# Optimization experiments

Hardware: AMD Instinct MI355X
Metric: run time of the kernel (lower is better)

## Reference

```python
import jax, jax.numpy as jnp
import numpy as np

S, B, C, HD = 3, 64, 256, 256
ZS, XS = 7, 31
EPS = 1e-5


def _bn(x, g, b, m, v):
    # inference-mode BatchNorm2d on NCHW
    inv = g / jnp.sqrt(v + EPS)
    return x * inv[None, :, None, None] + (b - m * inv)[None, :, None, None]


def _dw3(x, w):
    # depthwise 3x3 conv, VALID padding, groups = channels; w: [C,1,3,3]
    return jax.lax.conv_general_dilated(
        x, w, (1, 1), 'VALID', feature_group_count=x.shape[1],
        dimension_numbers=('NCHW', 'OIHW', 'NCHW'))


def _xcorr_depthwise(x, k):
    # Siamese depthwise cross-correlation: groups = batch*channels
    b, c, h, w = x.shape
    o = jax.lax.conv_general_dilated(
        x.reshape(1, b * c, h, w),
        k.reshape(b * c, 1, k.shape[2], k.shape[3]),
        (1, 1), 'VALID', feature_group_count=b * c,
        dimension_numbers=('NCHW', 'OIHW', 'NCHW'))
    return o.reshape(b, c, o.shape[2], o.shape[3])


def _c1(x, w):
    # 1x1 conv, no bias; w: [O,C]
    return jnp.einsum('bchw,oc->bohw', x, w)


def _forward(z_fs, x_fs, pre_w, pre_g, pre_b, pre_m, pre_v,
             head_w, head_g, head_b, head_m, head_v,
             cls_w1, cls_g, cls_b, cls_m, cls_v, cls_w2, cls_b2,
             loc_w1, loc_g, loc_b, loc_m, loc_v, loc_w2, loc_b2,
             ctr_w1, ctr_g, ctr_b, ctr_m, ctr_v, ctr_w2, ctr_b2,
             w_cls, w_loc, w_ctr):
    relu = jax.nn.relu
    cls_l, loc_l, ctr_l = [], [], []
    for i in range(S):
        search = relu(_bn(_dw3(x_fs[i], pre_w[i]), pre_g[i], pre_b[i], pre_m[i], pre_v[i]))
        kernel = relu(_bn(_dw3(z_fs[i], pre_w[i]), pre_g[i], pre_b[i], pre_m[i], pre_v[i]))
        feat = relu(_bn(_c1(_xcorr_depthwise(search, kernel), head_w[i]),
                        head_g[i], head_b[i], head_m[i], head_v[i]))

        def hd(w1, g, b, m, v, w2, b2):
            h = relu(_bn(_c1(feat, w1), g, b, m, v))
            return _c1(h, w2) + b2[None, :, None, None]

        cls_l.append(hd(cls_w1[i], cls_g[i], cls_b[i], cls_m[i], cls_v[i], cls_w2[i], cls_b2[i]))
        loc_l.append(hd(loc_w1[i], loc_g[i], loc_b[i], loc_m[i], loc_v[i], loc_w2[i], loc_b2[i]))
        ctr_l.append(hd(ctr_w1[i], ctr_g[i], ctr_b[i], ctr_m[i], ctr_v[i], ctr_w2[i], ctr_b2[i]))

    wc = jax.nn.softmax(w_cls)
    wl = jax.nn.softmax(w_loc)
    wt = jax.nn.softmax(w_ctr)
    cls = sum(cls_l[i] * wc[i] for i in range(S))
    loc = sum(loc_l[i] * wl[i] for i in range(S))
    ctr = sum(ctr_l[i] * wt[i] for i in range(S))
    return cls, loc, ctr


def setup_inputs() -> dict:
    key = jax.random.key(0)
    ks = iter(jax.random.split(key, 64))

    def rn(shape, scale=0.05):
        return jax.random.normal(next(ks), shape, jnp.float32) * scale

    def bn_params(n):
        return (jnp.ones((S, n), jnp.float32), jnp.zeros((S, n), jnp.float32),
                rn((S, n), 0.1), jax.random.uniform(next(ks), (S, n), jnp.float32) + 0.5)

    inp = {}
    inp['z_fs'] = rn((S, B, C, ZS, ZS), 1.0)
    inp['x_fs'] = rn((S, B, C, XS, XS), 1.0)
    inp['pre_w'] = rn((S, C, 1, 3, 3), 0.2)
    inp['pre_g'], inp['pre_b'], inp['pre_m'], inp['pre_v'] = bn_params(C)
    inp['head_w'] = rn((S, HD, C))
    inp['head_g'], inp['head_b'], inp['head_m'], inp['head_v'] = bn_params(HD)
    for nm, co in (('cls', 2), ('loc', 4), ('ctr', 1)):
        inp[nm + '_w1'] = rn((S, HD, HD))
        inp[nm + '_g'], inp[nm + '_b'], inp[nm + '_m'], inp[nm + '_v'] = bn_params(HD)
        inp[nm + '_w2'] = rn((S, co, HD))
        inp[nm + '_b2'] = jnp.zeros((S, co), jnp.float32)
    inp['w_cls'] = jnp.ones((S,), jnp.float32)
    inp['w_loc'] = jnp.ones((S,), jnp.float32)
    inp['w_ctr'] = jnp.ones((S,), jnp.float32)
    return inp


def reference(z_fs, x_fs, pre_w, pre_g, pre_b, pre_m, pre_v,
              head_w, head_g, head_b, head_m, head_v,
              cls_w1, cls_g, cls_b, cls_m, cls_v, cls_w2, cls_b2,
              loc_w1, loc_g, loc_b, loc_m, loc_v, loc_w2, loc_b2,
              ctr_w1, ctr_g, ctr_b, ctr_m, ctr_v, ctr_w2, ctr_b2,
              w_cls, w_loc, w_ctr):
    return _forward(z_fs, x_fs, pre_w, pre_g, pre_b, pre_m, pre_v,
                    head_w, head_g, head_b, head_m, head_v,
                    cls_w1, cls_g, cls_b, cls_m, cls_v, cls_w2, cls_b2,
                    loc_w1, loc_g, loc_b, loc_m, loc_v, loc_w2, loc_b2,
                    ctr_w1, ctr_g, ctr_b, ctr_m, ctr_v, ctr_w2, ctr_b2,
                    w_cls, w_loc, w_ctr)
```

## Files before the change

### kernel.cpp

```cpp
#include <hip/hip_runtime.h>
#include <hip/hip_bf16.h>

using bf16 = __hip_bfloat16;

#define B_  64
#define C_  256
#define HD_ 256
#define XS  31
#define XO  29
#define ZS  7
#define ZO  5
#define OSP 25
#define XO2 (XO*XO)
#define ZO2 (ZO*ZO)
#define OS2 (OSP*OSP)
#define EPSF 1e-5f

#define XCST 976
#define SRS  36
#define SCST (29 * SRS)

typedef __attribute__((ext_vector_type(4))) float f32x4;
typedef __attribute__((ext_vector_type(8))) short s16x8;

__device__ __forceinline__ unsigned short f2bf(float f) {
    union { float f; unsigned int u; } a; a.f = f;
    unsigned int r = a.u + 0x7FFF + ((a.u >> 16) & 1);
    return (unsigned short)(r >> 16);
}
__device__ __forceinline__ unsigned int pk2(unsigned short a, unsigned short b) {
    return (unsigned int)a | ((unsigned int)b << 16);
}

__global__ void wconv_k(const float* __restrict__ hw, const float* __restrict__ cw,
                        const float* __restrict__ lw, const float* __restrict__ tw,
                        unsigned short* __restrict__ o)
{
    int i = blockIdx.x * 256 + threadIdx.x;
    if (i >= 4 * 196608) return;
    int seg = i / 196608, r = i - seg * 196608;
    const float* s = (seg == 0) ? hw : (seg == 1) ? cw : (seg == 2) ? lw : tw;
    o[i] = f2bf(s[r]);
}

__global__ __launch_bounds__(256) void fused_pre_xcorr(
    const float* __restrict__ x, const float* __restrict__ z,
    const float* __restrict__ w, const float* __restrict__ g,
    const float* __restrict__ bb, const float* __restrict__ mm,
    const float* __restrict__ vv, unsigned short* __restrict__ out,
    int si_base)
{
    const int zs  = blockIdx.y;
    const int si  = si_base + zs;
    const int bc0 = blockIdx.x * 2;
    const int tid = threadIdx.x;

    __shared__ float xt[2 * XCST + 8];
    __shared__ float st[2 * SCST + 16];
    __shared__ float zt[2 * 49];
    __shared__ float ktl[2 * 25];
    __shared__ float wtl[2 * 9];
    __shared__ float sprm[4];

    const float* xp = x + ((size_t)si * B_ * C_ + bc0) * (XS * XS);
    #pragma unroll
    for (int k2 = 0; k2 < 8; ++k2) {
        int idx = tid + k2 * 256;
        if (idx < 2 * XS * XS) {
            int off = idx + (idx >= XS * XS ? (XCST - XS * XS) : 0);
            xt[off] = xp[idx];
        }
    }
    if (tid < 98) zt[tid] = z[((size_t)si * B_ * C_ + bc0) * 49 + tid];
    if (tid < 18) wtl[tid] = w[((size_t)si * C_ + (bc0 & (C_ - 1))) * 9 + tid];
    if (tid < 2) {
        int cg = si * C_ + (bc0 & (C_ - 1)) + tid;
        float iv = g[cg] * rsqrtf(vv[cg] + EPSF);
        sprm[tid * 2]     = iv;
        sprm[tid * 2 + 1] = bb[cg] - mm[cg] * iv;
    }
    __syncthreads();

    if (tid < 50) {
        int ch = (tid >= 25) ? 1 : 0;
        int l  = tid - ch * 25;
        int oy = l / 5, ox = l - (l / 5) * 5;
        const float* zb = &zt[ch * 49];
        const float* wb = &wtl[ch * 9];
        float a = 0.f;
        #pragma unroll
        for (int dy = 0; dy < 3; ++dy)
            #pragma unroll
            for (int dx = 0; dx < 3; ++dx)
                a += zb[(oy + dy) * ZS + ox + dx] * wb[dy * 3 + dx];
        ktl[ch * 25 + l] = fmaxf(a * sprm[ch * 2] + sprm[ch * 2 + 1], 0.f);
    }

    if (tid < 240) {
        int ch    = (tid >= 120) ? 1 : 0;
        int rem   = tid - ch * 120;
        int strip = rem >> 3;
        int cgp   = rem & 7;
        int r0    = strip * 2;
        const float* base = &xt[ch * XCST + r0 * XS + cgp * 4];
        const float* wb   = &wtl[ch * 9];
        float w0 = wb[0], w1 = wb[1], w2 = wb[2],
              w3 = wb[3], w4 = wb[4], w5 = wb[5],
              w6 = wb[6], w7 = wb[7], w8 = wb[8];
        const float inv  = sprm[ch * 2];
        const float beta = sprm[ch * 2 + 1];

        float a0 = 0.f, a1 = 0.f, a2 = 0.f, a3 = 0.f;
        float b0 = 0.f, b1 = 0.f, b2 = 0.f, b3 = 0.f;
        #pragma unroll
        for (int dy = 0; dy < 4; ++dy) {
            const float* rp = base + dy * XS;
            float v0 = rp[0], v1 = rp[1], v2 = rp[2],
                  v3 = rp[3], v4 = rp[4], v5 = rp[5];
            if (dy < 3) {
                float u0 = (dy == 0) ? w0 : (dy == 1) ? w3 : w6;
                float u1 = (dy == 0) ? w1 : (dy == 1) ? w4 : w7;
                float u2 = (dy == 0) ? w2 : (dy == 1) ? w5 : w8;
                a0 += v0 * u0 + v1 * u1 + v2 * u2;
                a1 += v1 * u0 + v2 * u1 + v3 * u2;
                a2 += v2 * u0 + v3 * u1 + v4 * u2;
                a3 += v3 * u0 + v4 * u1 + v5 * u2;
            }
            if (dy >= 1) {
                float u0 = (dy == 1) ? w0 : (dy == 2) ? w3 : w6;
                float u1 = (dy == 1) ? w1 : (dy == 2) ? w4 : w7;
                float u2 = (dy == 1) ? w2 : (dy == 2) ? w5 : w8;
                b0 += v0 * u0 + v1 * u1 + v2 * u2;
                b1 += v1 * u0 + v2 * u1 + v3 * u2;
                b2 += v2 * u0 + v3 * u1 + v4 * u2;
                b3 += v3 * u0 + v4 * u1 + v5 * u2;
            }
        }
        float4 ra;
        ra.x = fmaxf(a0 * inv + beta, 0.f);
        ra.y = fmaxf(a1 * inv + beta, 0.f);
        ra.z = fmaxf(a2 * inv + beta, 0.f);
        ra.w = fmaxf(a3 * inv + beta, 0.f);
        *(float4*)&st[ch * SCST + r0 * SRS + cgp * 4] = ra;
        if (r0 + 1 < XO) {
            float4 rb;
            rb.x = fmaxf(b0 * inv + beta, 0.f);
            rb.y = fmaxf(b1 * inv + beta, 0.f);
            rb.z = fmaxf(b2 * inv + beta, 0.f);
            rb.w = fmaxf(b3 * inv + beta, 0.f);
            *(float4*)&st[ch * SCST + (r0 + 1) * SRS + cgp * 4] = rb;
        }
    }
    __syncthreads();

    {
        const int ch = tid >> 7;
        const int l  = tid & 127;
        if (l < 125) {
            const float* kb = &ktl[ch * 25];
            float kt[25];
            #pragma unroll
            for (int j = 0; j < 25; ++j) kt[j] = kb[j];
            int u  = l / 5;
            int v0 = (l - u * 5) * 5;
            const float* sbase = &st[ch * SCST + u * SRS + v0];
            float o0 = 0.f, o1 = 0.f, o2 = 0.f, o3 = 0.f, o4 = 0.f;
            #pragma unroll
            for (int p = 0; p < 5; ++p) {
                const float* rp = sbase + p * SRS;
                float r0 = rp[0], r1 = rp[1], r2 = rp[2], r3 = rp[3], r4 = rp[4],
                      r5 = rp[5], r6 = rp[6], r7 = rp[7], r8 = rp[8];
                float k0 = kt[p * 5], k1 = kt[p * 5 + 1], k2 = kt[p * 5 + 2],
                      k3 = kt[p * 5 + 3], k4 = kt[p * 5 + 4];
                o0 += r0 * k0 + r1 * k1 + r2 * k2 + r3 * k3 + r4 * k4;
                o1 += r1 * k0 + r2 * k1 + r3 * k2 + r4 * k3 + r5 * k4;
                o2 += r2 * k0 + r3 * k1 + r4 * k2 + r5 * k3 + r6 * k4;
                o3 += r3 * k0 + r4 * k1 + r5 * k2 + r6 * k3 + r7 * k4;
                o4 += r4 * k0 + r5 * k1 + r6 * k2 + r7 * k3 + r8 * k4;
            }
            unsigned short* op = out + ((size_t)zs * B_ * C_ + bc0 + ch) * OS2
                                     + u * OSP + v0;
            op[0] = f2bf(o0); op[1] = f2bf(o1); op[2] = f2bf(o2);
            op[3] = f2bf(o3); op[4] = f2bf(o4);
        }
    }
}

__global__ __launch_bounds__(256) void c1_mfma(
    const unsigned short* __restrict__ X,
    const float* __restrict__ W,
    const unsigned short* __restrict__ Wbf,
    const float* __restrict__ g, const float* __restrict__ bb,
    const float* __restrict__ mm, const float* __restrict__ vv,
    unsigned short* __restrict__ out, int si_base)
{
    __shared__ unsigned short Abuf[4 * 128 * 8];
    __shared__ unsigned short Bbuf[4 * 128 * 8];
    __shared__ float s_inv[128], s_beta[128];

    const int tid  = threadIdx.x;
    const int wave = tid >> 6, lane = tid & 63;
    const int quad = lane >> 4, l16 = lane & 15;
    const int sb = blockIdx.x * 128;
    const int ob = blockIdx.y * 128;
    const int zs = blockIdx.z >> 6;
    const int si = si_base + zs;
    const int b  = blockIdx.z & 63;
    const int wm = (wave & 1) * 64, wn = (wave >> 1) * 64;

    const float* gs  = g  + (size_t)si * HD_;
    const float* bbs = bb + (size_t)si * HD_;
    const float* mms = mm + (size_t)si * HD_;
    const float* vvs = vv + (size_t)si * HD_;
    const float* Ws  = W  + (size_t)si * HD_ * C_;
    const unsigned short* Wbs = Wbf ? Wbf + (size_t)si * HD_ * C_ : nullptr;

    if (tid < 128) {
        int o = ob + tid;
        float iv = gs[o] * rsqrtf(vvs[o] + EPSF);
        s_inv[tid]  = iv;
        s_beta[tid] = bbs[o] - mms[o] * iv;
    }

    const int sm = tid & 127;
    const int kh = tid >> 7;
    const unsigned short* Xb = X + ((size_t)zs * B_ + b) * C_ * OS2;
    const bool npred = (sb + sm) < OS2;

    f32x4 acc[4][4];
    #pragma unroll
    for (int i = 0; i < 4; ++i)
        #pragma unroll
        for (int j = 0; j < 4; ++j)
            acc[i][j] = (f32x4){0.f, 0.f, 0.f, 0.f};

    for (int kk = 0; kk < C_; kk += 32) {
        uint4 pa0, pa1;
        if (Wbs) {
            const unsigned short* wp = Wbs + (size_t)(ob + sm) * C_ + kk + kh * 16;
            pa0 = *(const uint4*)(wp);
            pa1 = *(const uint4*)(wp + 8);
        } else {
            const float* wp = Ws + (size_t)(ob + sm) * C_ + kk + kh * 16;
            float4 w0 = *(const float4*)(wp + 0);
            float4 w1 = *(const float4*)(wp + 4);
            float4 w2 = *(const float4*)(wp + 8);
            float4 w3 = *(const float4*)(wp + 12);
            pa0.x = pk2(f2bf(w0.x), f2bf(w0.y)); pa0.y = pk2(f2bf(w0.z), f2bf(w0.w));
            pa0.z = pk2(f2bf(w1.x), f2bf(w1.y)); pa0.w = pk2(f2bf(w1.z), f2bf(w1.w));
            pa1.x = pk2(f2bf(w2.x), f2bf(w2.y)); pa1.y = pk2(f2bf(w2.z), f2bf(w2.w));
            pa1.z = pk2(f2bf(w3.x), f2bf(w3.y)); pa1.w = pk2(f2bf(w3.z), f2bf(w3.w));
        }
        *(uint4*)&Abuf[((kh * 2 + 0) * 128 + sm) * 8] = pa0;
        *(uint4*)&Abuf[((kh * 2 + 1) * 128 + sm) * 8] = pa1;

        unsigned short bu[16];
        #pragma unroll
        for (int j = 0; j < 16; ++j)
            bu[j] = npred ? Xb[(size_t)(kk + kh * 16 + j) * OS2 + sb + sm]
                          : (unsigned short)0;
        uint4 pb0, pb1;
        pb0.x = pk2(bu[0],  bu[1]);  pb0.y = pk2(bu[2],  bu[3]);
        pb0.z = pk2(bu[4],  bu[5]);  pb0.w = pk2(bu[6],  bu[7]);
        pb1.x = pk2(bu[8],  bu[9]);  pb1.y = pk2(bu[10], bu[11]);
        pb1.z = pk2(bu[12], bu[13]); pb1.w = pk2(bu[14], bu[15]);
        *(uint4*)&Bbuf[((kh * 2 + 0) * 128 + sm) * 8] = pb0;
        *(uint4*)&Bbuf[((kh * 2 + 1) * 128 + sm) * 8] = pb1;

        __syncthreads();

        s16x8 af[4], bfr[4];
        #pragma unroll
        for (int mt = 0; mt < 4; ++mt)
            af[mt] = *(const s16x8*)&Abuf[(quad * 128 + wm + mt * 16 + l16) * 8];
        #pragma unroll
        for (int nt = 0; nt < 4; ++nt)
            bfr[nt] = *(const s16x8*)&Bbuf[(quad * 128 + wn + nt * 16 + l16) * 8];
        #pragma unroll
        for (int mt = 0; mt < 4; ++mt)
            #pragma unroll
            for (int nt = 0; nt < 4; ++nt)
                acc[mt][nt] = __builtin_amdgcn_mfma_f32_16x16x32_bf16(
                    af[mt], bfr[nt], acc[mt][nt], 0, 0, 0);

        __syncthreads();
    }

    #pragma unroll
    for (int mt = 0; mt < 4; ++mt) {
        #pragma unroll
        for (int r = 0; r < 4; ++r) {
            int orow = wm + mt * 16 + quad * 4 + r;
            float iv = s_inv[orow], be = s_beta[orow];
            size_t obase = (((size_t)zs * B_ + b) * HD_ + (ob + orow)) * OS2;
            #pragma unroll
            for (int nt = 0; nt < 4; ++nt) {
                int s = sb + wn + nt * 16 + l16;
                if (s < OS2)
                    out[obase + s] = f2bf(fmaxf(acc[mt][nt][r] * iv + be, 0.f));
            }
        }
    }
}

__global__ __launch_bounds__(256) void heads3_mfma(
    const unsigned short* __restrict__ feat,
    const float* __restrict__ w1c, const float* __restrict__ w1l, const float* __restrict__ w1t,
    const unsigned short* __restrict__ Wbf,
    const float* __restrict__ gc, const float* __restrict__ bc2, const float* __restrict__ mc, const float* __restrict__ vc,
    const float* __restrict__ gl, const float* __restrict__ bl, const float* __restrict__ ml, const float* __restrict__ vl,
    const float* __restrict__ gt, const float* __restrict__ bt, const float* __restrict__ mt2, const float* __restrict__ vt,
    const float* __restrict__ w2c, const float* __restrict__ w2l, const float* __restrict__ w2t,
    const float* __restrict__ wvc, const float* __restrict__ wvl, const float* __restrict__ wvt,
    int si_base, float* __restrict__ oacc)
{
    __shared__ unsigned short Abuf[4 * 128 * 8];
    __shared__ unsigned short Bbuf[4 * 128 * 8];
    __shared__ float s_inv[128], s_beta[128];
    __shared__ float s_w2[4 * 256];

    const int tid  = threadIdx.x;
    const int wave = tid >> 6, lane = tid & 63;
    const int quad = lane >> 4, l16 = lane & 15;
    const int sb   = blockIdx.x * 128;
    const int by   = blockIdx.y;
    const int head = by >> 1;
    const int lob  = (by & 1) * 128;
    const int zs   = blockIdx.z >> 6;
    const int si   = si_base + zs;
    const int b    = blockIdx.z & 63;
    const int wm = (wave & 1) * 64, wn = (wave >> 1) * 64;

    const float* W  = (head == 0) ? w1c : (head == 1) ? w1l : w1t;
    const float* g  = (head == 0) ? gc  : (head == 1) ? gl  : gt;
    const float* bb = (head == 0) ? bc2 : (head == 1) ? bl  : bt;
    const float* mm = (head == 0) ? mc  : (head == 1) ? ml  : mt2;
    const float* vv = (head == 0) ? vc  : (head == 1) ? vl  : vt;
    const float* w2 = (head == 0) ? w2c : (head == 1) ? w2l : w2t;
    const float* wv = (head == 0) ? wvc : (head == 1) ? wvl : wvt;
    const int  CON  = (head == 0) ? 2 : (head == 1) ? 4 : 1;

    const float* Ws  = W + (size_t)si * HD_ * C_;
    const unsigned short* Wbs =
        Wbf ? Wbf + (size_t)(head + 1) * (3 * HD_ * C_) + (size_t)si * HD_ * C_ : nullptr;
    g  += (size_t)si * HD_;  bb += (size_t)si * HD_;
    mm += (size_t)si * HD_;  vv += (size_t)si * HD_;
    w2 += (size_t)si * CON * HD_;

    if (tid < 128) {
        int o = lob + tid;
        float iv = g[o] * rsqrtf(vv[o] + EPSF);
        s_inv[tid]  = iv;
        s_beta[tid] = bb[o] - mm[o] * iv;
    }
    for (int t = tid; t < CON * 256; t += 256) s_w2[t] = w2[t];

    const int sm = tid & 127;
    const int kh = tid >> 7;
    const unsigned short* Xb = feat + ((size_t)zs * B_ + b) * C_ * OS2;
    const bool npred = (sb + sm) < OS2;

    f32x4 acc[4][4];
    #pragma unroll
    for (int i = 0; i < 4; ++i)
        #pragma unroll
        for (int j = 0; j < 4; ++j)
            acc[i][j] = (f32x4){0.f, 0.f, 0.f, 0.f};

    for (int kk = 0; kk < C_; kk += 32) {
        uint4 pa0, pa1;
        if (Wbs) {
            const unsigned short* wp = Wbs + (size_t)(lob + sm) * C_ + kk + kh * 16;
            pa0 = *(const uint4*)(wp);
            pa1 = *(const uint4*)(wp + 8);
        } else {
            const float* wp = Ws + (size_t)(lob + sm) * C_ + kk + kh * 16;
            float4 w0 = *(const float4*)(wp + 0);
            float4 w1 = *(const float4*)(wp + 4);
            float4 w2v4 = *(const float4*)(wp + 8);
            float4 w3 = *(const float4*)(wp + 12);
            pa0.x = pk2(f2bf(w0.x), f2bf(w0.y)); pa0.y = pk2(f2bf(w0.z), f2bf(w0.w));
            pa0.z = pk2(f2bf(w1.x), f2bf(w1.y)); pa0.w = pk2(f2bf(w1.z), f2bf(w1.w));
            pa1.x = pk2(f2bf(w2v4.x), f2bf(w2v4.y)); pa1.y = pk2(f2bf(w2v4.z), f2bf(w2v4.w));
            pa1.z = pk2(f2bf(w3.x), f2bf(w3.y)); pa1.w = pk2(f2bf(w3.z), f2bf(w3.w));
        }
        *(uint4*)&Abuf[((kh * 2 + 0) * 128 + sm) * 8] = pa0;
        *(uint4*)&Abuf[((kh * 2 + 1) * 128 + sm) * 8] = pa1;

        unsigned short bu[16];
        #pragma unroll
        for (int j = 0; j < 16; ++j)
            bu[j] = npred ? Xb[(size_t)(kk + kh * 16 + j) * OS2 + sb + sm]
                          : (unsigned short)0;
        uint4 pb0, pb1;
        pb0.x = pk2(bu[0],  bu[1]);  pb0.y = pk2(bu[2],  bu[3]);
        pb0.z = pk2(bu[4],  bu[5]);  pb0.w = pk2(bu[6],  bu[7]);
        pb1.x = pk2(bu[8],  bu[9]);  pb1.y = pk2(bu[10], bu[11]);
        pb1.z = pk2(bu[12], bu[13]); pb1.w = pk2(bu[14], bu[15]);
        *(uint4*)&Bbuf[((kh * 2 + 0) * 128 + sm) * 8] = pb0;
        *(uint4*)&Bbuf[((kh * 2 + 1) * 128 + sm) * 8] = pb1;

        __syncthreads();

        s16x8 af[4], bfr[4];
        #pragma unroll
        for (int mt = 0; mt < 4; ++mt)
            af[mt] = *(const s16x8*)&Abuf[(quad * 128 + wm + mt * 16 + l16) * 8];
        #pragma unroll
        for (int nt = 0; nt < 4; ++nt)
            bfr[nt] = *(const s16x8*)&Bbuf[(quad * 128 + wn + nt * 16 + l16) * 8];
        #pragma unroll
        for (int mt = 0; mt < 4; ++mt)
            #pragma unroll
            for (int nt = 0; nt < 4; ++nt)
                acc[mt][nt] = __builtin_amdgcn_mfma_f32_16x16x32_bf16(
                    af[mt], bfr[nt], acc[mt][nt], 0, 0, 0);

        __syncthreads();
    }

    #pragma unroll
    for (int mt = 0; mt < 4; ++mt)
        #pragma unroll
        for (int r = 0; r < 4; ++r) {
            int orow = wm + mt * 16 + quad * 4 + r;
            float iv = s_inv[orow], be = s_beta[orow];
            #pragma unroll
            for (int nt = 0; nt < 4; ++nt)
                acc[mt][nt][r] = fmaxf(acc[mt][nt][r] * iv + be, 0.f);
        }

    const float e0 = __expf(wv[0]), e1 = __expf(wv[1]), e2 = __expf(wv[2]);
    const float wi = ((si == 0) ? e0 : (si == 1) ? e1 : e2) / (e0 + e1 + e2);

    float* obase;
    if (head == 0)      obase = oacc + (size_t)b * 2 * OS2;
    else if (head == 1) obase = oacc + (size_t)B_ * 2 * OS2 + (size_t)b * 4 * OS2;
    else                obase = oacc + (size_t)B_ * 6 * OS2 + (size_t)b * OS2;

    for (int co = 0; co < CON; ++co) {
        float red[4] = {0.f, 0.f, 0.f, 0.f};
        #pragma unroll
        for (int mt = 0; mt < 4; ++mt)
            #pragma unroll
            for (int r = 0; r < 4; ++r) {
                float w2v = s_w2[co * 256 + lob + wm + mt * 16 + quad * 4 + r];
                #pragma unroll
                for (int nt = 0; nt < 4; ++nt)
                    red[nt] += w2v * acc[mt][nt][r];
            }
        #pragma unroll
        for (int nt = 0; nt < 4; ++nt) {
            red[nt] += __shfl_xor(red[nt], 16);
            red[nt] += __shfl_xor(red[nt], 32);
        }
        if (quad == 0) {
            #pragma unroll
            for (int nt = 0; nt < 4; ++nt) {
                int s = sb + wn + nt * 16 + l16;
                if (s < OS2)
                    atomicAdd(obase + (size_t)co * OS2 + s, wi * red[nt]);
            }
        }
    }
}

__global__ void bias_out(float* __restrict__ out,
    const float* __restrict__ cb2, const float* __restrict__ lb2,
    const float* __restrict__ tb2, const float* __restrict__ wvc,
    const float* __restrict__ wvl, const float* __restrict__ wvt)
{
    int n = blockIdx.x * 256 + threadIdx.x;
    if (n >= B_ * 7 * OS2) return;
    float bias;
    if (n < B_ * 2 * OS2) {
        float e0 = __expf(wvc[0]), e1 = __expf(wvc[1]), e2 = __expf(wvc[2]);
        int co = (n / OS2) & 1;
        bias = (e0 * cb2[co] + e1 * cb2[2 + co] + e2 * cb2[4 + co]) / (e0 + e1 + e2);
    } else if (n < B_ * 6 * OS2) {
        float e0 = __expf(wvl[0]), e1 = __expf(wvl[1]), e2 = __expf(wvl[2]);
        int co = ((n - B_ * 2 * OS2) / OS2) & 3;
        bias = (e0 * lb2[co] + e1 * lb2[4 + co] + e2 * lb2[8 + co]) / (e0 + e1 + e2);
    } else {
        float e0 = __expf(wvt[0]), e1 = __expf(wvt[1]), e2 = __expf(wvt[2]);
        bias = (e0 * tb2[0] + e1 * tb2[1] + e2 * tb2[2]) / (e0 + e1 + e2);
    }
    out[n] += bias;
}

__global__ void fillf_k(float* __restrict__ out, int n, float v)
{
    int i = blockIdx.x * 256 + threadIdx.x;
    if (i < n) out[i] = v;
}

extern "C" void kernel_launch(void* const* d_in, const int* in_sizes, int n_in,
                              void* d_out, int out_size, void* d_ws, size_t ws_size,
                              hipStream_t stream)
{
    static const int EXP_SIZES[36] = {
        2408448, 47235072, 6912,
        768, 768, 768, 768,
        196608, 768, 768, 768, 768,
        196608, 768, 768, 768, 768, 1536, 6,
        196608, 768, 768, 768, 768, 3072, 12,
        196608, 768, 768, 768, 768, 768, 3,
        3, 3, 3
    };
    int bad = -1;
    if (n_in != 36) bad = 99;
    else {
        for (int i = 0; i < 36; ++i)
            if (in_sizes[i] != EXP_SIZES[i]) { bad = i; break; }
    }
    if (bad < 0 && ws_size < (size_t)40960000) bad = 90;
    if (bad < 0 && out_size != 280000) bad = 95;
    if (bad >= 0) {
        fillf_k<<<(out_size + 255) / 256, 256, 0, stream>>>(
            (float*)d_out, out_size, 500.f + 4.f * bad);
        return;
    }

    const float* z_fs   = (const float*)d_in[0];
    const float* x_fs   = (const float*)d_in[1];
    const float* pre_w  = (const float*)d_in[2];
    const float* pre_g  = (const float*)d_in[3];
    const float* pre_b  = (const float*)d_in[4];
    const float* pre_m  = (const float*)d_in[5];
    const float* pre_v  = (const float*)d_in[6];
    const float* head_w = (const float*)d_in[7];
    const float* head_g = (const float*)d_in[8];
    const float* head_b = (const float*)d_in[9];
    const float* head_m = (const float*)d_in[10];
    const float* head_v = (const float*)d_in[11];
    const float* cls_w1 = (const float*)d_in[12];
    const float* cls_g  = (const float*)d_in[13];
    const float* cls_b  = (const float*)d_in[14];
    const float* cls_m  = (const float*)d_in[15];
    const float* cls_v  = (const float*)d_in[16];
    const float* cls_w2 = (const float*)d_in[17];
    const float* cls_b2 = (const float*)d_in[18];
    const float* loc_w1 = (const float*)d_in[19];
    const float* loc_g  = (const float*)d_in[20];
    const float* loc_b  = (const float*)d_in[21];
    const float* loc_m  = (const float*)d_in[22];
    const float* loc_v  = (const float*)d_in[23];
    const float* loc_w2 = (const float*)d_in[24];
    const float* loc_b2 = (const float*)d_in[25];
    const float* ctr_w1 = (const float*)d_in[26];
    const float* ctr_g  = (const float*)d_in[27];
    const float* ctr_b  = (const float*)d_in[28];
    const float* ctr_m  = (const float*)d_in[29];
    const float* ctr_v  = (const float*)d_in[30];
    const float* ctr_w2 = (const float*)d_in[31];
    const float* ctr_b2 = (const float*)d_in[32];
    const float* w_cls  = (const float*)d_in[33];
    const float* w_loc  = (const float*)d_in[34];
    const float* w_ctr  = (const float*)d_in[35];

    const int OUT_N = B_ * 7 * OS2;
    const size_t stageEl = (size_t)B_ * C_ * OS2;
    const size_t WBF_EL = (size_t)4 * 3 * HD_ * C_;
    const bool batched = ws_size >= (6 * stageEl + WBF_EL) * sizeof(unsigned short);

    hipMemsetAsync(d_out, 0, (size_t)OUT_N * sizeof(float), stream);

    if (batched) {
        unsigned short* xc   = (unsigned short*)d_ws;
        unsigned short* feat = xc + 3 * stageEl;
        unsigned short* wbf  = feat + 3 * stageEl;

        wconv_k<<<(4 * 196608 + 255) / 256, 256, 0, stream>>>(
            head_w, cls_w1, loc_w1, ctr_w1, wbf);

        fused_pre_xcorr<<<dim3(B_ * C_ / 2, 3), 256, 0, stream>>>(
            x_fs, z_fs, pre_w, pre_g, pre_b, pre_m, pre_v, xc, 0);

        c1_mfma<<<dim3(5, 2, 3 * B_), 256, 0, stream>>>(
            xc, head_w, wbf, head_g, head_b, head_m, head_v, feat, 0);

        heads3_mfma<<<dim3(5, 6, 3 * B_), 256, 0, stream>>>(
            feat, cls_w1, loc_w1, ctr_w1, wbf,
            cls_g, cls_b, cls_m, cls_v,
            loc_g, loc_b, loc_m, loc_v,
            ctr_g, ctr_b, ctr_m, ctr_v,
            cls_w2, loc_w2, ctr_w2,
            w_cls, w_loc, w_ctr, 0, (float*)d_out);
    } else {
        unsigned short* xc   = (unsigned short*)d_ws;
        unsigned short* feat = xc + stageEl;

        for (int i = 0; i < 3; ++i) {
            fused_pre_xcorr<<<dim3(B_ * C_ / 2, 1), 256, 0, stream>>>(
                x_fs, z_fs, pre_w, pre_g, pre_b, pre_m, pre_v, xc, i);

            c1_mfma<<<dim3(5, 2, B_), 256, 0, stream>>>(
                xc, head_w, nullptr, head_g, head_b, head_m, head_v, feat, i);

            heads3_mfma<<<dim3(5, 6, B_), 256, 0, stream>>>(
                feat, cls_w1, loc_w1, ctr_w1, nullptr,
                cls_g, cls_b, cls_m, cls_v,
                loc_g, loc_b, loc_m, loc_v,
                ctr_g, ctr_b, ctr_m, ctr_v,
                cls_w2, loc_w2, ctr_w2,
                w_cls, w_loc, w_ctr, i, (float*)d_out);
        }
    }

    bias_out<<<(OUT_N + 255) / 256, 256, 0, stream>>>(
        (float*)d_out, cls_b2, loc_b2, ctr_b2, w_cls, w_loc, w_ctr);
}
```

Measured before the change: 564.0 us.

## Stage full-K activation tile in LDS once and loop all output tiles per block

Both 1x1-conv GEMM kernels now load the entire K=256 activation slab for a 128-column spatial tile into shared memory once, then iterate over all output-row tiles (2 for the head conv, 6 for the three branch heads) with weights read directly from global bf16. This removes the repeated strided gathers of the activation tensor across grid.y blocks and the per-K-step barriers. In exchange, grid size shrinks 2x/6x, LDS use grows to 64KB per block (lowering occupancy), and weight fragments are fetched from global/L2 with no LDS staging. The non-batched fallback path is removed and the workspace requirement is enforced up front.

```diff
diff --git a/kernel.cpp b/kernel.cpp
--- a/kernel.cpp
+++ b/kernel.cpp
@@ -188,38 +188,32 @@
 
 __global__ __launch_bounds__(256) void c1_mfma(
     const unsigned short* __restrict__ X,
-    const float* __restrict__ W,
     const unsigned short* __restrict__ Wbf,
     const float* __restrict__ g, const float* __restrict__ bb,
     const float* __restrict__ mm, const float* __restrict__ vv,
-    unsigned short* __restrict__ out, int si_base)
-{
-    __shared__ unsigned short Abuf[4 * 128 * 8];
-    __shared__ unsigned short Bbuf[4 * 128 * 8];
-    __shared__ float s_inv[128], s_beta[128];
+    unsigned short* __restrict__ out)
+{
+    __shared__ unsigned short Bsh[32 * 128 * 8];
+    __shared__ float s_inv[256], s_beta[256];
 
     const int tid  = threadIdx.x;
     const int wave = tid >> 6, lane = tid & 63;
     const int quad = lane >> 4, l16 = lane & 15;
     const int sb = blockIdx.x * 128;
-    const int ob = blockIdx.y * 128;
-    const int zs = blockIdx.z >> 6;
-    const int si = si_base + zs;
-    const int b  = blockIdx.z & 63;
+    const int zs = blockIdx.y >> 6;
+    const int b  = blockIdx.y & 63;
     const int wm = (wave & 1) * 64, wn = (wave >> 1) * 64;
 
-    const float* gs  = g  + (size_t)si * HD_;
-    const float* bbs = bb + (size_t)si * HD_;
-    const float* mms = mm + (size_t)si * HD_;
-    const float* vvs = vv + (size_t)si * HD_;
-    const float* Ws  = W  + (size_t)si * HD_ * C_;
-    const unsigned short* Wbs = Wbf ? Wbf + (size_t)si * HD_ * C_ : nullptr;
-
-    if (tid < 128) {
-        int o = ob + tid;
-        float iv = gs[o] * rsqrtf(vvs[o] + EPSF);
+    const float* gs  = g  + (size_t)zs * HD_;
+    const float* bbs = bb + (size_t)zs * HD_;
+    const float* mms = mm + (size_t)zs * HD_;
+    const float* vvs = vv + (size_t)zs * HD_;
+    const unsigned short* wA0 = Wbf + (size_t)zs * HD_ * C_;
+
+    {
+        float iv = gs[tid] * rsqrtf(vvs[tid] + EPSF);
         s_inv[tid]  = iv;
-        s_beta[tid] = bbs[o] - mms[o] * iv;
+        s_beta[tid] = bbs[tid] - mms[tid] * iv;
     }
 
     const int sm = tid & 127;
@@ -227,77 +221,65 @@
     const unsigned short* Xb = X + ((size_t)zs * B_ + b) * C_ * OS2;
     const bool npred = (sb + sm) < OS2;
 
-    f32x4 acc[4][4];
     #pragma unroll
-    for (int i = 0; i < 4; ++i)
-        #pragma unroll
-        for (int j = 0; j < 4; ++j)
-            acc[i][j] = (f32x4){0.f, 0.f, 0.f, 0.f};
-
-    for (int kk = 0; kk < C_; kk += 32) {
-        uint4 pa0, pa1;
-        if (Wbs) {
-            const unsigned short* wp = Wbs + (size_t)(ob + sm) * C_ + kk + kh * 16;
-            pa0 = *(const uint4*)(wp);
-            pa1 = *(const uint4*)(wp + 8);
-        } else {
-            const float* wp = Ws + (size_t)(ob + sm) * C_ + kk + kh * 16;
-            float4 w0 = *(const float4*)(wp + 0);
-            float4 w1 = *(const float4*)(wp + 4);
-            float4 w2 = *(const float4*)(wp + 8);
-            float4 w3 = *(const float4*)(wp + 12);
-            pa0.x = pk2(f2bf(w0.x), f2bf(w0.y)); pa0.y = pk2(f2bf(w0.z), f2bf(w0.w));
-            pa0.z = pk2(f2bf(w1.x), f2bf(w1.y)); pa0.w = pk2(f2bf(w1.z), f2bf(w1.w));
-            pa1.x = pk2(f2bf(w2.x), f2bf(w2.y)); pa1.y = pk2(f2bf(w2.z), f2bf(w2.w));
-            pa1.z = pk2(f2bf(w3.x), f2bf(w3.y)); pa1.w = pk2(f2bf(w3.z), f2bf(w3.w));
-        }
-        *(uint4*)&Abuf[((kh * 2 + 0) * 128 + sm) * 8] = pa0;
-        *(uint4*)&Abuf[((kh * 2 + 1) * 128 + sm) * 8] = pa1;
-
+    for (int kk = 0; kk < 8; ++kk) {
         unsigned short bu[16];
         #pragma unroll
         for (int j = 0; j < 16; ++j)
-            bu[j] = npred ? Xb[(size_t)(kk + kh * 16 + j) * OS2 + sb + sm]
+            bu[j] = npred ? Xb[(size_t)(kk * 32 + kh * 16 + j) * OS2 + sb + sm]
                           : (unsigned short)0;
         uint4 pb0, pb1;
         pb0.x = pk2(bu[0],  bu[1]);  pb0.y = pk2(bu[2],  bu[3]);
         pb0.z = pk2(bu[4],  bu[5]);  pb0.w = pk2(bu[6],  bu[7]);
         pb1.x = pk2(bu[8],  bu[9]);  pb1.y = pk2(bu[10], bu[11]);
         pb1.z = pk2(bu[12], bu[13]); pb1.w = pk2(bu[14], bu[15]);
-        *(uint4*)&Bbuf[((kh * 2 + 0) * 128 + sm) * 8] = pb0;
-        *(uint4*)&Bbuf[((kh * 2 + 1) * 128 + sm) * 8] = pb1;
-
-        __syncthreads();
-
-        s16x8 af[4], bfr[4];
-        #pragma unroll
-        for (int mt = 0; mt < 4; ++mt)
-            af[mt] = *(const s16x8*)&Abuf[(quad * 128 + wm + mt * 16 + l16) * 8];
-        #pragma unroll
-        for (int nt = 0; nt < 4; ++nt)
-            bfr[nt] = *(const s16x8*)&Bbuf[(quad * 128 + wn + nt * 16 + l16) * 8];
-        #pragma unroll
-        for (int mt = 0; mt < 4; ++mt)
+        int kq0 = kk * 4 + kh * 2;
+        *(uint4*)&Bsh[((kq0 + 0) * 128 + sm) * 8] = pb0;
+        *(uint4*)&Bsh[((kq0 + 1) * 128 + sm) * 8] = pb1;
+    }
+    __syncthreads();
+
+    #pragma unroll
+    for (int mtile = 0; mtile < 2; ++mtile) {
+        const int ob = mtile * 128;
+        f32x4 acc[4][4];
+        #pragma unroll
+        for (int i = 0; i < 4; ++i)
+            #pragma unroll
+            for (int j = 0; j < 4; ++j)
+                acc[i][j] = (f32x4){0.f, 0.f, 0.f, 0.f};
+
+        for (int kc = 0; kc < 8; ++kc) {
+            s16x8 af[4], bfr[4];
+            #pragma unroll
+            for (int mt = 0; mt < 4; ++mt) {
+                int row = ob + wm + mt * 16 + l16;
+                af[mt] = *(const s16x8*)&wA0[(size_t)row * C_ + kc * 32 + quad * 8];
+            }
             #pragma unroll
             for (int nt = 0; nt < 4; ++nt)
-                acc[mt][nt] = __builtin_amdgcn_mfma_f32_16x16x32_bf16(
-                    af[mt], bfr[nt], acc[mt][nt], 0, 0, 0);
-
-        __syncthreads();
-    }
-
-    #pragma unroll
-    for (int mt = 0; mt < 4; ++mt) {
-        #pragma unroll
-        for (int r = 0; r < 4; ++r) {
-            int orow = wm + mt * 16 + quad * 4 + r;
-            float iv = s_inv[orow], be = s_beta[orow];
-            size_t obase = (((size_t)zs * B_ + b) * HD_ + (ob + orow)) * OS2;
-            #pragma unroll
-            for (int nt = 0; nt < 4; ++nt) {
-                int s = sb + wn + nt * 16 + l16;
-                if (s < OS2)
-                    out[obase + s] = f2bf(fmaxf(acc[mt][nt][r] * iv + be, 0.f));
+                bfr[nt] = *(const s16x8*)&Bsh[((kc * 4 + quad) * 128 + wn + nt * 16 + l16) * 8];
+            #pragma unroll
+            for (int mt = 0; mt < 4; ++mt)
+                #pragma unroll
+                for (int nt = 0; nt < 4; ++nt)
+                    acc[mt][nt] = __builtin_amdgcn_mfma_f32_16x16x32_bf16(
+                        af[mt], bfr[nt], acc[mt][nt], 0, 0, 0);
+        }
+
+        #pragma unroll
+        for (int mt = 0; mt < 4; ++mt) {
+            #pragma unroll
+            for (int r = 0; r < 4; ++r) {
+                int orow = ob + wm + mt * 16 + quad * 4 + r;
+                float iv = s_inv[orow], be = s_beta[orow];
+                size_t obase = (((size_t)zs * B_ + b) * HD_ + orow) * OS2;
+                #pragma unroll
+                for (int nt = 0; nt < 4; ++nt) {
+                    int s = sb + wn + nt * 16 + l16;
+                    if (s < OS2)
+                        out[obase + s] = f2bf(fmaxf(acc[mt][nt][r] * iv + be, 0.f));
+                }
             }
         }
     }
@@ -305,161 +287,154 @@
 
 __global__ __launch_bounds__(256) void heads3_mfma(
     const unsigned short* __restrict__ feat,
-    const float* __restrict__ w1c, const float* __restrict__ w1l, const float* __restrict__ w1t,
     const unsigned short* __restrict__ Wbf,
     const float* __restrict__ gc, const float* __restrict__ bc2, const float* __restrict__ mc, const float* __restrict__ vc,
     const float* __restrict__ gl, const float* __restrict__ bl, const float* __restrict__ ml, const float* __restrict__ vl,
     const float* __restrict__ gt, const float* __restrict__ bt, const float* __restrict__ mt2, const float* __restrict__ vt,
     const float* __restrict__ w2c, const float* __restrict__ w2l, const float* __restrict__ w2t,
     const float* __restrict__ wvc, const float* __restrict__ wvl, const float* __restrict__ wvt,
-    int si_base, float* __restrict__ oacc)
-{
-    __shared__ unsigned short Abuf[4 * 128 * 8];
-    __shared__ unsigned short Bbuf[4 * 128 * 8];
-    __shared__ float s_inv[128], s_beta[128];
-    __shared__ float s_w2[4 * 256];
+    float* __restrict__ oacc)
+{
+    __shared__ unsigned short Bsh[32 * 128 * 8];
+    __shared__ float s_inv[3 * 256], s_beta[3 * 256];
+    __shared__ float s_w2[7 * 256];
 
     const int tid  = threadIdx.x;
     const int wave = tid >> 6, lane = tid & 63;
     const int quad = lane >> 4, l16 = lane & 15;
-    const int sb   = blockIdx.x * 128;
-    const int by   = blockIdx.y;
-    const int head = by >> 1;
-    const int lob  = (by & 1) * 128;
-    const int zs   = blockIdx.z >> 6;
-    const int si   = si_base + zs;
-    const int b    = blockIdx.z & 63;
+    const int sb = blockIdx.x * 128;
+    const int zs = blockIdx.y >> 6;
+    const int b  = blockIdx.y & 63;
     const int wm = (wave & 1) * 64, wn = (wave >> 1) * 64;
 
-    const float* W  = (head == 0) ? w1c : (head == 1) ? w1l : w1t;
-    const float* g  = (head == 0) ? gc  : (head == 1) ? gl  : gt;
-    const float* bb = (head == 0) ? bc2 : (head == 1) ? bl  : bt;
-    const float* mm = (head == 0) ? mc  : (head == 1) ? ml  : mt2;
-    const float* vv = (head == 0) ? vc  : (head == 1) ? vl  : vt;
-    const float* w2 = (head == 0) ? w2c : (head == 1) ? w2l : w2t;
-    const float* wv = (head == 0) ? wvc : (head == 1) ? wvl : wvt;
-    const int  CON  = (head == 0) ? 2 : (head == 1) ? 4 : 1;
-
-    const float* Ws  = W + (size_t)si * HD_ * C_;
-    const unsigned short* Wbs =
-        Wbf ? Wbf + (size_t)(head + 1) * (3 * HD_ * C_) + (size_t)si * HD_ * C_ : nullptr;
-    g  += (size_t)si * HD_;  bb += (size_t)si * HD_;
-    mm += (size_t)si * HD_;  vv += (size_t)si * HD_;
-    w2 += (size_t)si * CON * HD_;
-
-    if (tid < 128) {
-        int o = lob + tid;
-        float iv = g[o] * rsqrtf(vv[o] + EPSF);
-        s_inv[tid]  = iv;
-        s_beta[tid] = bb[o] - mm[o] * iv;
-    }
-    for (int t = tid; t < CON * 256; t += 256) s_w2[t] = w2[t];
+    {
+        float iv0 = gc[zs * HD_ + tid] * rsqrtf(vc[zs * HD_ + tid] + EPSF);
+        s_inv[tid]        = iv0;
+        s_beta[tid]       = bc2[zs * HD_ + tid] - mc[zs * HD_ + tid] * iv0;
+        float iv1 = gl[zs * HD_ + tid] * rsqrtf(vl[zs * HD_ + tid] + EPSF);
+        s_inv[256 + tid]  = iv1;
+        s_beta[256 + tid] = bl[zs * HD_ + tid] - ml[zs * HD_ + tid] * iv1;
+        float iv2 = gt[zs * HD_ + tid] * rsqrtf(vt[zs * HD_ + tid] + EPSF);
+        s_inv[512 + tid]  = iv2;
+        s_beta[512 + tid] = bt[zs * HD_ + tid] - mt2[zs * HD_ + tid] * iv2;
+    }
+    {
+        s_w2[tid]       = w2c[zs * 512 + tid];
+        s_w2[256 + tid] = w2c[zs * 512 + 256 + tid];
+        #pragma unroll
+        for (int q = 0; q < 4; ++q)
+            s_w2[512 + q * 256 + tid] = w2l[zs * 1024 + q * 256 + tid];
+        s_w2[1536 + tid] = w2t[zs * 256 + tid];
+    }
 
     const int sm = tid & 127;
     const int kh = tid >> 7;
     const unsigned short* Xb = feat + ((size_t)zs * B_ + b) * C_ * OS2;
     const bool npred = (sb + sm) < OS2;
 
-    f32x4 acc[4][4];
     #pragma unroll
-    for (int i = 0; i < 4; ++i)
-        #pragma unroll
-        for (int j = 0; j < 4; ++j)
-            acc[i][j] = (f32x4){0.f, 0.f, 0.f, 0.f};
-
-    for (int kk = 0; kk < C_; kk += 32) {
-        uint4 pa0, pa1;
-        if (Wbs) {
-            const unsigned short* wp = Wbs + (size_t)(lob + sm) * C_ + kk + kh * 16;
-            pa0 = *(const uint4*)(wp);
-            pa1 = *(const uint4*)(wp + 8);
-        } else {
-            const float* wp = Ws + (size_t)(lob + sm) * C_ + kk + kh * 16;
-            float4 w0 = *(const float4*)(wp + 0);
-            float4 w1 = *(const float4*)(wp + 4);
-            float4 w2v4 = *(const float4*)(wp + 8);
-            float4 w3 = *(const float4*)(wp + 12);
-            pa0.x = pk2(f2bf(w0.x), f2bf(w0.y)); pa0.y = pk2(f2bf(w0.z), f2bf(w0.w));
-            pa0.z = pk2(f2bf(w1.x), f2bf(w1.y)); pa0.w = pk2(f2bf(w1.z), f2bf(w1.w));
-            pa1.x = pk2(f2bf(w2v4.x), f2bf(w2v4.y)); pa1.y = pk2(f2bf(w2v4.z), f2bf(w2v4.w));
-            pa1.z = pk2(f2bf(w3.x), f2bf(w3.y)); pa1.w = pk2(f2bf(w3.z), f2bf(w3.w));
-        }
-        *(uint4*)&Abuf[((kh * 2 + 0) * 128 + sm) * 8] = pa0;
-        *(uint4*)&Abuf[((kh * 2 + 1) * 128 + sm) * 8] = pa1;
-
+    for (int kk = 0; kk < 8; ++kk) {
         unsigned short bu[16];
         #pragma unroll
         for (int j = 0; j < 16; ++j)
-            bu[j] = npred ? Xb[(size_t)(kk + kh * 16 + j) * OS2 + sb + sm]
+            bu[j] = npred ? Xb[(size_t)(kk * 32 + kh * 16 + j) * OS2 + sb + sm]
                           : (unsigned short)0;
         uint4 pb0, pb1;
         pb0.x = pk2(bu[0],  bu[1]);  pb0.y = pk2(bu[2],  bu[3]);
         pb0.z = pk2(bu[4],  bu[5]);  pb0.w = pk2(bu[6],  bu[7]);
         pb1.x = pk2(bu[8],  bu[9]);  pb1.y = pk2(bu[10], bu[11]);
         pb1.z = pk2(bu[12], bu[13]); pb1.w = pk2(bu[14], bu[15]);
-        *(uint4*)&Bbuf[((kh * 2 + 0) * 128 + sm) * 8] = pb0;
-        *(uint4*)&Bbuf[((kh * 2 + 1) * 128 + sm) * 8] = pb1;
-
-        __syncthreads();
-
-        s16x8 af[4], bfr[4];
-        #pragma unroll
-        for (int mt = 0; mt < 4; ++mt)
-            af[mt] = *(const s16x8*)&Abuf[(quad * 128 + wm + mt * 16 + l16) * 8];
-        #pragma unroll
-        for (int nt = 0; nt < 4; ++nt)
-            bfr[nt] = *(const s16x8*)&Bbuf[(quad * 128 + wn + nt * 16 + l16) * 8];
-        #pragma unroll
-        for (int mt = 0; mt < 4; ++mt)
+        int kq0 = kk * 4 + kh * 2;
+        *(uint4*)&Bsh[((kq0 + 0) * 128 + sm) * 8] = pb0;
+        *(uint4*)&Bsh[((kq0 + 1) * 128 + sm) * 8] = pb1;
+    }
+    __syncthreads();
+
+    float wih[3];
+    {
+        float e0 = __expf(wvc[0]), e1 = __expf(wvc[1]), e2 = __expf(wvc[2]);
+        wih[0] = ((zs == 0) ? e0 : (zs == 1) ? e1 : e2) / (e0 + e1 + e2);
+        float f0 = __expf(wvl[0]), f1 = __expf(wvl[1]), f2 = __expf(wvl[2]);
+        wih[1] = ((zs == 0) ? f0 : (zs == 1) ? f1 : f2) / (f0 + f1 + f2);
+        float h0 = __expf(wvt[0]), h1 = __expf(wvt[1]), h2 = __expf(wvt[2]);
+        wih[2] = ((zs == 0) ? h0 : (zs == 1) ? h1 : h2) / (h0 + h1 + h2);
+    }
+
+    for (int mtile = 0; mtile < 6; ++mtile) {
+        const int head = mtile >> 1;
+        const int lob  = (mtile & 1) * 128;
+        const unsigned short* wA =
+            Wbf + (size_t)(head + 1) * (3 * HD_ * C_) + (size_t)zs * HD_ * C_;
+
+        f32x4 acc[4][4];
+        #pragma unroll
+        for (int i = 0; i < 4; ++i)
+            #pragma unroll
+            for (int j = 0; j < 4; ++j)
+                acc[i][j] = (f32x4){0.f, 0.f, 0.f, 0.f};
+
+        for (int kc = 0; kc < 8; ++kc) {
+            s16x8 af[4], bfr[4];
+            #pragma unroll
+            for (int mt = 0; mt < 4; ++mt) {
+                int row = lob + wm + mt * 16 + l16;
+                af[mt] = *(const s16x8*)&wA[(size_t)row * C_ + kc * 32 + quad * 8];
+            }
             #pragma unroll
             for (int nt = 0; nt < 4; ++nt)
-                acc[mt][nt] = __builtin_amdgcn_mfma_f32_16x16x32_bf16(
-                    af[mt], bfr[nt], acc[mt][nt], 0, 0, 0);
-
-        __syncthreads();
-    }
-
-    #pragma unroll
-    for (int mt = 0; mt < 4; ++mt)
-        #pragma unroll
-        for (int r = 0; r < 4; ++r) {
-            int orow = wm + mt * 16 + quad * 4 + r;
-            float iv = s_inv[orow], be = s_beta[orow];
-            #pragma unroll
-            for (int nt = 0; nt < 4; ++nt)
-                acc[mt][nt][r] = fmaxf(acc[mt][nt][r] * iv + be, 0.f);
-        }
-
-    const float e0 = __expf(wv[0]), e1 = __expf(wv[1]), e2 = __expf(wv[2]);
-    const float wi = ((si == 0) ? e0 : (si == 1) ? e1 : e2) / (e0 + e1 + e2);
-
-    float* obase;
-    if (head == 0)      obase = oacc + (size_t)b * 2 * OS2;
-    else if (head == 1) obase = oacc + (size_t)B_ * 2 * OS2 + (size_t)b * 4 * OS2;
-    else                obase = oacc + (size_t)B_ * 6 * OS2 + (size_t)b * OS2;
-
-    for (int co = 0; co < CON; ++co) {
-        float red[4] = {0.f, 0.f, 0.f, 0.f};
-        #pragma unroll
-        for (int mt = 0; mt < 4; ++mt)
-            #pragma unroll
-            for (int r = 0; r < 4; ++r) {
-                float w2v = s_w2[co * 256 + lob + wm + mt * 16 + quad * 4 + r];
+                bfr[nt] = *(const s16x8*)&Bsh[((kc * 4 + quad) * 128 + wn + nt * 16 + l16) * 8];
+            #pragma unroll
+            for (int mt = 0; mt < 4; ++mt)
                 #pragma unroll
                 for (int nt = 0; nt < 4; ++nt)
-                    red[nt] += w2v * acc[mt][nt][r];
-            }
-        #pragma unroll
-        for (int nt = 0; nt < 4; ++nt) {
-            red[nt] += __shfl_xor(red[nt], 16);
-            red[nt] += __shfl_xor(red[nt], 32);
-        }
-        if (quad == 0) {
+                    acc[mt][nt] = __builtin_amdgcn_mfma_f32_16x16x32_bf16(
+                        af[mt], bfr[nt], acc[mt][nt], 0, 0, 0);
+        }
+
+        #pragma unroll
+        for (int mt = 0; mt < 4; ++mt)
+            #pragma unroll
+            for (int r = 0; r < 4; ++r) {
+                int orow = lob + wm + mt * 16 + quad * 4 + r;
+                float iv = s_inv[head * 256 + orow];
+                float be = s_beta[head * 256 + orow];
+                #pragma unroll
+                for (int nt = 0; nt < 4; ++nt)
+                    acc[mt][nt][r] = fmaxf(acc[mt][nt][r] * iv + be, 0.f);
+            }
+
+        const int CON   = (head == 0) ? 2 : (head == 1) ? 4 : 1;
+        const int w2off = (head == 0) ? 0 : (head == 1) ? 512 : 1536;
+        const float wi  = wih[head];
+
+        float* obase;
+        if (head == 0)      obase = oacc + (size_t)b * 2 * OS2;
+        else if (head == 1) obase = oacc + (size_t)B_ * 2 * OS2 + (size_t)b * 4 * OS2;
+        else                obase = oacc + (size_t)B_ * 6 * OS2 + (size_t)b * OS2;
+
+        for (int co = 0; co < CON; ++co) {
+            float red[4] = {0.f, 0.f, 0.f, 0.f};
+            #pragma unroll
+            for (int mt = 0; mt < 4; ++mt)
+                #pragma unroll
+                for (int r = 0; r < 4; ++r) {
+                    float w2v = s_w2[w2off + co * 256 + lob + wm + mt * 16 + quad * 4 + r];
+                    #pragma unroll
+                    for (int nt = 0; nt < 4; ++nt)
+                        red[nt] += w2v * acc[mt][nt][r];
+                }
             #pragma unroll
             for (int nt = 0; nt < 4; ++nt) {
-                int s = sb + wn + nt * 16 + l16;
-                if (s < OS2)
-                    atomicAdd(obase + (size_t)co * OS2 + s, wi * red[nt]);
+                red[nt] += __shfl_xor(red[nt], 16);
+                red[nt] += __shfl_xor(red[nt], 32);
+            }
+            if (quad == 0) {
+                #pragma unroll
+                for (int nt = 0; nt < 4; ++nt) {
+                    int s = sb + wn + nt * 16 + l16;
+                    if (s < OS2)
+                        atomicAdd(obase + (size_t)co * OS2 + s, wi * red[nt]);
+                }
             }
         }
     }
@@ -507,13 +482,18 @@
         196608, 768, 768, 768, 768, 768, 3,
         3, 3, 3
     };
+    const int OUT_N = B_ * 7 * OS2;
+    const size_t stageEl = (size_t)B_ * C_ * OS2;
+    const size_t WBF_EL  = (size_t)4 * 3 * HD_ * C_;
+    const size_t NEED_WS = (6 * stageEl + WBF_EL) * sizeof(unsigned short);
+
     int bad = -1;
     if (n_in != 36) bad = 99;
     else {
         for (int i = 0; i < 36; ++i)
             if (in_sizes[i] != EXP_SIZES[i]) { bad = i; break; }
     }
-    if (bad < 0 && ws_size < (size_t)40960000) bad = 90;
+    if (bad < 0 && ws_size < NEED_WS) bad = 90;
     if (bad < 0 && out_size != 280000) bad = 95;
     if (bad >= 0) {
         fillf_k<<<(out_size + 255) / 256, 256, 0, stream>>>(
@@ -558,54 +538,28 @@
     const float* w_loc  = (const float*)d_in[34];
     const float* w_ctr  = (const float*)d_in[35];
 
-    const int OUT_N = B_ * 7 * OS2;
-    const size_t stageEl = (size_t)B_ * C_ * OS2;
-    const size_t WBF_EL = (size_t)4 * 3 * HD_ * C_;
-    const bool batched = ws_size >= (6 * stageEl + WBF_EL) * sizeof(unsigned short);
+    unsigned short* xc   = (unsigned short*)d_ws;
+    unsigned short* feat = xc + 3 * stageEl;
+    unsigned short* wbf  = feat + 3 * stageEl;
 
     hipMemsetAsync(d_out, 0, (size_t)OUT_N * sizeof(float), stream);
 
-    if (batched) {
-        unsigned short* xc   = (unsigned short*)d_ws;
-        unsigned short* feat = xc + 3 * stageEl;
-        unsigned short* wbf  = feat + 3 * stageEl;
-
-        wconv_k<<<(4 * 196608 + 255) / 256, 256, 0, stream>>>(
-            head_w, cls_w1, loc_w1, ctr_w1, wbf);
-
-        fused_pre_xcorr<<<dim3(B_ * C_ / 2, 3), 256, 0, stream>>>(
-            x_fs, z_fs, pre_w, pre_g, pre_b, pre_m, pre_v, xc, 0);
-
-        c1_mfma<<<dim3(5, 2, 3 * B_), 256, 0, stream>>>(
-            xc, head_w, wbf, head_g, head_b, head_m, head_v, feat, 0);
-
-        heads3_mfma<<<dim3(5, 6, 3 * B_), 256, 0, stream>>>(
-            feat, cls_w1, loc_w1, ctr_w1, wbf,
-            cls_g, cls_b, cls_m, cls_v,
-            loc_g, loc_b, loc_m, loc_v,
-            ctr_g, ctr_b, ctr_m, ctr_v,
-            cls_w2, loc_w2, ctr_w2,
-            w_cls, w_loc, w_ctr, 0, (float*)d_out);
-    } else {
-        unsigned short* xc   = (unsigned short*)d_ws;
-        unsigned short* feat = xc + stageEl;
-
-        for (int i = 0; i < 3; ++i) {
-            fused_pre_xcorr<<<dim3(B_ * C_ / 2, 1), 256, 0, stream>>>(
-                x_fs, z_fs, pre_w, pre_g, pre_b, pre_m, pre_v, xc, i);
-
-            c1_mfma<<<dim3(5, 2, B_), 256, 0, stream>>>(
-                xc, head_w, nullptr, head_g, head_b, head_m, head_v, feat, i);
-
-            heads3_mfma<<<dim3(5, 6, B_), 256, 0, stream>>>(
-                feat, cls_w1, loc_w1, ctr_w1, nullptr,
-                cls_g, cls_b, cls_m, cls_v,
-                loc_g, loc_b, loc_m, loc_v,
-                ctr_g, ctr_b, ctr_m, ctr_v,
-                cls_w2, loc_w2, ctr_w2,
-                w_cls, w_loc, w_ctr, i, (float*)d_out);
-        }
-    }
+    wconv_k<<<(4 * 196608 + 255) / 256, 256, 0, stream>>>(
+        head_w, cls_w1, loc_w1, ctr_w1, wbf);
+
+    fused_pre_xcorr<<<dim3(B_ * C_ / 2, 3), 256, 0, stream>>>(
+        x_fs, z_fs, pre_w, pre_g, pre_b, pre_m, pre_v, xc, 0);
+
+    c1_mfma<<<dim3(5, 3 * B_), 256, 0, stream>>>(
+        xc, wbf, head_g, head_b, head_m, head_v, feat);
+
+    heads3_mfma<<<dim3(5, 3 * B_), 256, 0, stream>>>(
+        feat, wbf,
+        cls_g, cls_b, cls_m, cls_v,
+        loc_g, loc_b, loc_m, loc_v,
+        ctr_g, ctr_b, ctr_m, ctr_v,
+        cls_w2, loc_w2, ctr_w2,
+        w_cls, w_loc, w_ctr, (float*)d_out);
 
     bias_out<<<(OUT_N + 255) / 256, 256, 0, stream>>>(
         (float*)d_out, cls_b2, loc_b2, ctr_b2, w_cls, w_loc, w_ctr);
```

Result: slower. 602.9 us (+6.9%).
